# Kernel tuning notes

Measured on AMD Instinct MI355X. Metric: run time of the kernel, lower is better.

## Reference

```python
import jax, jax.numpy as jnp
import numpy as np

# network config (matches init_kwargs)
NI, NT, NA = 128, 3584, 384          # input / transmission / action neurons
N = NI + NT + NA                      # 4096 total neurons
HID, KQ, SIG = 32, 16, 16             # neuron_hidden_dim, key_query_dim, signal_dim
IN_DIM, OUT_DIM = 128, 64
B, T = 64, 32


def setup_inputs() -> dict:
    key = jax.random.key(0)
    ks = jax.random.split(key, 10)
    s = 0.1
    return {
        "x": jax.random.normal(ks[0], (B, T, IN_DIM), dtype=jnp.float32),
        # input neurons: MLP input_size -> HID -> SIG, stacked over NI neurons
        "W1_in": jax.random.normal(ks[1], (NI, HID, IN_DIM)) * s,
        "b1_in": jnp.zeros((NI, HID)),
        "W2_in": jax.random.normal(ks[2], (NI, SIG, HID)) * s,
        "b2_in": jnp.zeros((NI, SIG)),
        # transmission + action neurons: MLP SIG -> HID -> SIG, stacked over NT+NA
        "W1_o": jax.random.normal(ks[3], (NT + NA, HID, SIG)) * s,
        "b1_o": jnp.zeros((NT + NA, HID)),
        "W2_o": jax.random.normal(ks[4], (NT + NA, SIG, HID)) * s,
        "b2_o": jnp.zeros((NT + NA, SIG)),
        # per-neuron learned query / key vectors (broadcast over batch in original)
        "q_all": jax.random.normal(ks[5], (N, KQ)) * s,
        "k_all": jax.random.normal(ks[6], (N, KQ)) * s,
        # action projection: (NA*SIG) -> OUT_DIM
        "Wp": jax.random.normal(ks[7], (OUT_DIM, NA * SIG)) * s,
        "bp": jnp.zeros((OUT_DIM,)),
    }


def reference(x, W1_in, b1_in, W2_in, b2_in, W1_o, b1_o, W2_o, b2_o,
              q_all, k_all, Wp, bp):
    # attention weights are batch-independent (q/k are per-neuron params),
    # identical every step -> compute once. [N, N], softmax over keys.
    scores = (q_all @ k_all.T) / jnp.sqrt(jnp.asarray(KQ, x.dtype))
    attn = jax.nn.softmax(scores, axis=-1)

    def step(prev, x_t):
        # prev: [B, N, SIG]; aggregate messages from all neurons' previous outputs
        ctx = jnp.einsum('nm,bmd->bnd', attn, prev)              # [B, N, SIG]
        # input neurons all see the raw external input x_t
        h_in = jnp.tanh(jnp.einsum('bi,nhi->bnh', x_t, W1_in) + b1_in)
        out_in = jnp.einsum('bnh,ndh->bnd', h_in, W2_in) + b2_in  # [B, NI, SIG]
        # transmission + action neurons consume their attention context
        h_o = jnp.tanh(jnp.einsum('bns,nhs->bnh', ctx[:, NI:, :], W1_o) + b1_o)
        out_o = jnp.einsum('bnh,ndh->bnd', h_o, W2_o) + b2_o      # [B, NT+NA, SIG]
        new = jnp.concatenate([out_in, out_o], axis=1)            # [B, N, SIG]
        act = new[:, NI + NT:, :].reshape(x_t.shape[0], NA * SIG)
        y = act @ Wp.T + bp                                       # [B, OUT_DIM]
        return new, y

    prev0 = jnp.zeros((x.shape[0], N, SIG), dtype=x.dtype)
    _, ys = jax.lax.scan(step, prev0, jnp.swapaxes(x, 0, 1))      # [T, B, OUT]
    return jnp.swapaxes(ys, 0, 1)                                 # [B, T, OUT]
```

## Files before the change

kernel.cpp:

```cpp
#include <hip/hip_runtime.h>
#include <hip/hip_bf16.h>


#define NI 128
#define NTR 3584
#define NA 384
#define NN 4096
#define NO (NN - NI)
#define HID 32
#define KQ 16
#define SIG 16
#define IN_DIM 128
#define OUT_DIM 64
#define BB 64
#define TT 32
#define CDIM (BB * SIG)

#define BM 128
#define BN 128
#define BK 32
#define CTXP 132

typedef unsigned short ushort_t;
typedef __attribute__((ext_vector_type(8))) short short8v;
typedef __attribute__((ext_vector_type(4))) float f32x4;

__device__ inline ushort_t f2b(float f) {
  __hip_bfloat16 h = __float2bfloat16(f);
  return *reinterpret_cast<ushort_t*>(&h);
}

__device__ inline float tanh_fast(float s) {
  const float e = __expf(2.f * s);
  return 1.f - 2.f / (e + 1.f);
}

__device__ inline void gll16(const void* g, void* l) {
  __builtin_amdgcn_global_load_lds(
      (const __attribute__((address_space(1))) unsigned int*)g,
      (__attribute__((address_space(3))) unsigned int*)l, 16, 0, 0);
}

__global__ __launch_bounds__(256) void attn_kernel(const float* __restrict__ q_all,
                                                   const float* __restrict__ k_all,
                                                   ushort_t* __restrict__ A) {
  const int row = blockIdx.x;
  const int n = NI + row;
  float q[KQ];
#pragma unroll
  for (int i = 0; i < KQ; ++i) q[i] = q_all[n * KQ + i];

  float e[16];
  float local = 0.f;
#pragma unroll
  for (int j = 0; j < 16; ++j) {
    const int m = j * 256 + threadIdx.x;
    const float* kr = k_all + (size_t)m * KQ;
    float s = 0.f;
#pragma unroll
    for (int i = 0; i < KQ; ++i) s += q[i] * kr[i];
    e[j] = __expf(s * 0.25f);
    local += e[j];
  }
  __shared__ float red[256];
  red[threadIdx.x] = local;
  __syncthreads();
  for (int off = 128; off > 0; off >>= 1) {
    if (threadIdx.x < off) red[threadIdx.x] += red[threadIdx.x + off];
    __syncthreads();
  }
  const float inv = 1.f / red[0];
#pragma unroll
  for (int j = 0; j < 16; ++j) {
    const int m = j * 256 + threadIdx.x;
    A[(size_t)row * NN + m] = f2b(e[j] * inv);
  }
}

__global__ __launch_bounds__(256) void fused_step_kernel(
    const ushort_t* __restrict__ A,
    const ushort_t* __restrict__ Bst,
    const float* __restrict__ x, int t,
    const float* __restrict__ W1_in, const float* __restrict__ b1_in,
    const float* __restrict__ W2_in, const float* __restrict__ b2_in,
    const float* __restrict__ W1_o, const float* __restrict__ b1_o,
    const float* __restrict__ W2_o, const float* __restrict__ b2_o,
    ushort_t* __restrict__ STnext,
    float* __restrict__ act) {
  __shared__ ushort_t As[BM * BK];
  __shared__ ushort_t Bs[BN * BK];
  __shared__ float ctxs[128 * CTXP];

  const int tid = threadIdx.x;
  const int bx = blockIdx.x, by = blockIdx.y;
  const int nbase = by * BN;

  if (bx < 31) {
    const int mbase = bx * BM;
    const int wave = tid >> 6, lane = tid & 63;
    const int wr = wave >> 1, wc = wave & 1;

    f32x4 acc[4][4];
#pragma unroll
    for (int i = 0; i < 4; ++i)
#pragma unroll
      for (int j = 0; j < 4; ++j) acc[i][j] = (f32x4){0.f, 0.f, 0.f, 0.f};

    const int row0 = tid >> 2;
    const int k0 = (tid & 3) * 8;
    const ushort_t* ga0 = A + (size_t)(mbase + row0) * NN + k0;
    const ushort_t* ga1 = ga0 + (size_t)64 * NN;
    const ushort_t* gb0 = Bst + (size_t)(nbase + row0) * NN + k0;
    const ushort_t* gb1 = gb0 + (size_t)64 * NN;
    ushort_t* laA0 = As + wave * 512;
    ushort_t* laA1 = As + 2048 + wave * 512;
    ushort_t* laB0 = Bs + wave * 512;
    ushort_t* laB1 = Bs + 2048 + wave * 512;

    const int r = lane & 15, koff = (lane >> 4) * 8;

    for (int ks = 0; ks < NN / BK; ++ks) {
      __syncthreads();
      gll16(ga0, laA0); gll16(ga1, laA1);
      gll16(gb0, laB0); gll16(gb1, laB1);
      ga0 += BK; ga1 += BK; gb0 += BK; gb1 += BK;
      __syncthreads();

      short8v a[4], b[4];
#pragma unroll
      for (int mi = 0; mi < 4; ++mi)
        a[mi] = *(const short8v*)&As[(wr * 64 + mi * 16 + r) * BK + koff];
#pragma unroll
      for (int ni = 0; ni < 4; ++ni)
        b[ni] = *(const short8v*)&Bs[(wc * 64 + ni * 16 + r) * BK + koff];
#pragma unroll
      for (int mi = 0; mi < 4; ++mi)
#pragma unroll
        for (int ni = 0; ni < 4; ++ni)
          acc[mi][ni] = __builtin_amdgcn_mfma_f32_16x16x32_bf16(a[mi], b[ni], acc[mi][ni], 0, 0, 0);
    }

    const int r4 = (lane >> 4) * 4, cidx = lane & 15;
#pragma unroll
    for (int mi = 0; mi < 4; ++mi)
#pragma unroll
      for (int ni = 0; ni < 4; ++ni)
#pragma unroll
        for (int v = 0; v < 4; ++v)
          ctxs[(wr * 64 + mi * 16 + r4 + v) * CTXP + wc * 64 + ni * 16 + cidx] = acc[mi][ni][v];
    __syncthreads();

    const bool is_action = (mbase >= 3584);
    for (int iter = 0; iter < 4; ++iter) {
      const int nr = iter * 32 + (tid >> 3);
      const int bl = tid & 7;
      float cv[SIG];
      const float* cp = ctxs + nr * CTXP + bl * SIG;
#pragma unroll
      for (int d = 0; d < SIG; ++d) cv[d] = cp[d];

      const int no = mbase + nr;
      const float* w1 = W1_o + (size_t)no * HID * SIG;
      const float* b1 = b1_o + (size_t)no * HID;
      float h[HID];
#pragma unroll
      for (int hh = 0; hh < HID; ++hh) {
        float s = b1[hh];
#pragma unroll
        for (int d = 0; d < SIG; ++d) s += w1[hh * SIG + d] * cv[d];
        h[hh] = tanh_fast(s);
      }
      const float* w2 = W2_o + (size_t)no * SIG * HID;
      const float* b2 = b2_o + (size_t)no * SIG;
      float o16[SIG];
#pragma unroll
      for (int d = 0; d < SIG; ++d) {
        float s = b2[d];
#pragma unroll
        for (int hh = 0; hh < HID; ++hh) s += w2[d * HID + hh] * h[hh];
        o16[d] = s;
      }
      if (is_action) {
        float* ap = act + (size_t)(by * 8 + bl) * (NA * SIG) + (size_t)(no - 3584) * SIG;
#pragma unroll
        for (int k = 0; k < 4; ++k)
          *(float4*)(ap + 4 * k) = make_float4(o16[4*k], o16[4*k+1], o16[4*k+2], o16[4*k+3]);
      }
      float* wp = ctxs + nr * CTXP + bl * SIG;
#pragma unroll
      for (int d = 0; d < SIG; ++d) wp[d] = o16[d];
    }
    __syncthreads();
  } else {
    for (int iter = 0; iter < 4; ++iter) {
      const int nr = iter * 32 + (tid >> 3);
      const int bl = tid & 7;
      const int bg = by * 8 + bl;
      const float* xb = x + ((size_t)bg * TT + t) * IN_DIM;
      const float* w1 = W1_in + (size_t)nr * HID * IN_DIM;
      float h[HID];
#pragma unroll
      for (int hh = 0; hh < HID; ++hh) h[hh] = b1_in[nr * HID + hh];
      for (int i = 0; i < IN_DIM; i += 4) {
        const float4 xv = *(const float4*)(xb + i);
#pragma unroll
        for (int hh = 0; hh < HID; ++hh) {
          const float4 wv = *(const float4*)(w1 + hh * IN_DIM + i);
          h[hh] += wv.x * xv.x + wv.y * xv.y + wv.z * xv.z + wv.w * xv.w;
        }
      }
#pragma unroll
      for (int hh = 0; hh < HID; ++hh) h[hh] = tanh_fast(h[hh]);
      const float* w2 = W2_in + (size_t)nr * SIG * HID;
      float o16[SIG];
#pragma unroll
      for (int d = 0; d < SIG; ++d) {
        float s = b2_in[nr * SIG + d];
#pragma unroll
        for (int hh = 0; hh < HID; ++hh) s += w2[d * HID + hh] * h[hh];
        o16[d] = s;
      }
      float* wp = ctxs + nr * CTXP + bl * SIG;
#pragma unroll
      for (int d = 0; d < SIG; ++d) wp[d] = o16[d];
    }
    __syncthreads();
  }

  const int col0 = (bx == 31) ? 0 : NI + bx * BM;
  const int c = tid >> 1, nh = tid & 1;
  const float* colp = ctxs + (size_t)nh * 64 * CTXP + c;
  uint4* dst = (uint4*)(STnext + (size_t)(nbase + c) * NN + col0 + nh * 64);
#pragma unroll
  for (int k = 0; k < 8; ++k) {
    const unsigned w0 = (unsigned)f2b(colp[(k*8+0)*CTXP]) | ((unsigned)f2b(colp[(k*8+1)*CTXP]) << 16);
    const unsigned w1 = (unsigned)f2b(colp[(k*8+2)*CTXP]) | ((unsigned)f2b(colp[(k*8+3)*CTXP]) << 16);
    const unsigned w2 = (unsigned)f2b(colp[(k*8+4)*CTXP]) | ((unsigned)f2b(colp[(k*8+5)*CTXP]) << 16);
    const unsigned w3 = (unsigned)f2b(colp[(k*8+6)*CTXP]) | ((unsigned)f2b(colp[(k*8+7)*CTXP]) << 16);
    dst[k] = make_uint4(w0, w1, w2, w3);
  }
}

__global__ __launch_bounds__(256) void proj_kernel(const float* __restrict__ act,
                                                   const float* __restrict__ Wp,
                                                   const float* __restrict__ bp,
                                                   float* __restrict__ out, int t) {
  const int b = blockIdx.x;
  const int o = threadIdx.x & 63, q = threadIdx.x >> 6;
  const float* a = act + (size_t)b * (NA * SIG) + q * 1536;
  const float* w = Wp + (size_t)o * (NA * SIG) + q * 1536;
  float s = 0.f;
  for (int j = 0; j < 1536; j += 4) {
    const float4 av = *(const float4*)(a + j);
    const float4 wv = *(const float4*)(w + j);
    s += av.x * wv.x + av.y * wv.y + av.z * wv.z + av.w * wv.w;
  }
  __shared__ float red[4][64];
  red[q][o] = s;
  __syncthreads();
  if (q == 0) {
    const float y = red[0][o] + red[1][o] + red[2][o] + red[3][o] + bp[o];
    out[((size_t)b * TT + t) * OUT_DIM + o] = y;
  }
}

extern "C" void kernel_launch(void* const* d_in, const int* in_sizes, int n_in,
                              void* d_out, int out_size, void* d_ws, size_t ws_size,
                              hipStream_t stream) {
  const float* x     = (const float*)d_in[0];
  const float* W1_in = (const float*)d_in[1];
  const float* b1_in = (const float*)d_in[2];
  const float* W2_in = (const float*)d_in[3];
  const float* b2_in = (const float*)d_in[4];
  const float* W1_o  = (const float*)d_in[5];
  const float* b1_o  = (const float*)d_in[6];
  const float* W2_o  = (const float*)d_in[7];
  const float* b2_o  = (const float*)d_in[8];
  const float* q_all = (const float*)d_in[9];
  const float* k_all = (const float*)d_in[10];
  const float* Wp    = (const float*)d_in[11];
  const float* bp    = (const float*)d_in[12];
  float* out = (float*)d_out;

  char* p = (char*)d_ws;
  ushort_t* Abf = (ushort_t*)p; p += (size_t)NO * NN * 2;
  ushort_t* ST0 = (ushort_t*)p; p += (size_t)CDIM * NN * 2;
  ushort_t* ST1 = (ushort_t*)p; p += (size_t)CDIM * NN * 2;
  float*    act = (float*)p;    p += (size_t)BB * NA * SIG * 4;

  hipMemsetAsync(ST0, 0, (size_t)CDIM * NN * 2, stream);
  attn_kernel<<<NO, 256, 0, stream>>>(q_all, k_all, Abf);

  for (int t = 0; t < TT; ++t) {
    ushort_t* prev = (t & 1) ? ST1 : ST0;
    ushort_t* next = (t & 1) ? ST0 : ST1;
    dim3 grid(32, CDIM / BN);
    fused_step_kernel<<<grid, 256, 0, stream>>>(Abf, prev, x, t,
                                                W1_in, b1_in, W2_in, b2_in,
                                                W1_o, b1_o, W2_o, b2_o, next, act);
    proj_kernel<<<BB, 256, 0, stream>>>(act, Wp, bp, out, t);
  }
}
```

Measured before the change: 6.901 ms.

## Double-buffer GEMM K-tiles with swizzled LDS and transpose Wp for coalesced projection

The main GEMM loop now uses BK=64 with two LDS buffers, issuing the next tile's global-to-LDS loads before computing on the current one, so there is one barrier per step instead of two. Loads use an XOR swizzle on the k offset to reduce LDS bank conflicts. Separately, Wp is transposed once into workspace so the projection kernel reads weights coalesced across output lanes. In exchange, LDS use grows, with the ctx buffer plus double buffers at about 130KB, which may lower occupancy or exceed the limit.

```diff
diff --git a/kernel.cpp b/kernel.cpp
--- a/kernel.cpp
+++ b/kernel.cpp
@@ -18,7 +18,8 @@
 
 #define BM 128
 #define BN 128
-#define BK 32
+#define BK 64
+#define NKS (NN / BK)
 #define CTXP 132
 
 typedef unsigned short ushort_t;
@@ -75,6 +76,20 @@
     const int m = j * 256 + threadIdx.x;
     A[(size_t)row * NN + m] = f2b(e[j] * inv);
   }
+}
+
+__global__ __launch_bounds__(256) void wpt_kernel(const float* __restrict__ Wp,
+                                                  float* __restrict__ WpT) {
+  __shared__ float tile[64][65];
+  const int j0 = blockIdx.x * 64;
+  const int tx = threadIdx.x & 63, ty = threadIdx.x >> 6;
+#pragma unroll
+  for (int oo = ty; oo < 64; oo += 4)
+    tile[oo][tx] = Wp[(size_t)oo * (NA * SIG) + j0 + tx];
+  __syncthreads();
+#pragma unroll
+  for (int oo = ty; oo < 64; oo += 4)
+    WpT[(size_t)(j0 + oo) * 64 + tx] = tile[tx][oo];
 }
 
 __global__ __launch_bounds__(256) void fused_step_kernel(
@@ -87,8 +102,8 @@
     const float* __restrict__ W2_o, const float* __restrict__ b2_o,
     ushort_t* __restrict__ STnext,
     float* __restrict__ act) {
-  __shared__ ushort_t As[BM * BK];
-  __shared__ ushort_t Bs[BN * BK];
+  __shared__ ushort_t Abuf[2][BM * BK];
+  __shared__ ushort_t Bbuf[2][BN * BK];
   __shared__ float ctxs[128 * CTXP];
 
   const int tid = threadIdx.x;
@@ -99,6 +114,7 @@
     const int mbase = bx * BM;
     const int wave = tid >> 6, lane = tid & 63;
     const int wr = wave >> 1, wc = wave & 1;
+    const int r = lane & 15, hi = lane >> 4;
 
     f32x4 acc[4][4];
 #pragma unroll
@@ -106,41 +122,58 @@
 #pragma unroll
       for (int j = 0; j < 4; ++j) acc[i][j] = (f32x4){0.f, 0.f, 0.f, 0.f};
 
-    const int row0 = tid >> 2;
-    const int k0 = (tid & 3) * 8;
-    const ushort_t* ga0 = A + (size_t)(mbase + row0) * NN + k0;
-    const ushort_t* ga1 = ga0 + (size_t)64 * NN;
-    const ushort_t* gb0 = Bst + (size_t)(nbase + row0) * NN + k0;
-    const ushort_t* gb1 = gb0 + (size_t)64 * NN;
-    ushort_t* laA0 = As + wave * 512;
-    ushort_t* laA1 = As + 2048 + wave * 512;
-    ushort_t* laB0 = Bs + wave * 512;
-    ushort_t* laB1 = Bs + 2048 + wave * 512;
-
-    const int r = lane & 15, koff = (lane >> 4) * 8;
-
-    for (int ks = 0; ks < NN / BK; ++ks) {
-      __syncthreads();
-      gll16(ga0, laA0); gll16(ga1, laA1);
-      gll16(gb0, laB0); gll16(gb1, laB1);
-      ga0 += BK; ga1 += BK; gb0 += BK; gb1 += BK;
-      __syncthreads();
-
-      short8v a[4], b[4];
+    const int trow = tid >> 3;
+    const int k0 = ((tid & 7) ^ (trow & 7)) << 3;
+    const ushort_t* sa[4];
+    const ushort_t* sb[4];
+#pragma unroll
+    for (int c = 0; c < 4; ++c) {
+      sa[c] = A   + (size_t)(mbase + c * 32 + trow) * NN + k0;
+      sb[c] = Bst + (size_t)(nbase + c * 32 + trow) * NN + k0;
+    }
+    const int ldst = tid * 8;
+
+#pragma unroll
+    for (int c = 0; c < 4; ++c) {
+      gll16(sa[c], &Abuf[0][c * 2048 + ldst]);
+      gll16(sb[c], &Bbuf[0][c * 2048 + ldst]);
+      sa[c] += BK; sb[c] += BK;
+    }
+
+    for (int ks = 0; ks < NKS; ++ks) {
+      const int cur = ks & 1;
+      asm volatile("s_waitcnt vmcnt(0)" ::: "memory");
+      __builtin_amdgcn_s_barrier();
+      if (ks + 1 < NKS) {
+#pragma unroll
+        for (int c = 0; c < 4; ++c) {
+          gll16(sa[c], &Abuf[cur ^ 1][c * 2048 + ldst]);
+          gll16(sb[c], &Bbuf[cur ^ 1][c * 2048 + ldst]);
+          sa[c] += BK; sb[c] += BK;
+        }
+        asm volatile("" ::: "memory");
+      }
+
+      short8v a[4][2], b[4][2];
 #pragma unroll
       for (int mi = 0; mi < 4; ++mi)
-        a[mi] = *(const short8v*)&As[(wr * 64 + mi * 16 + r) * BK + koff];
-#pragma unroll
-      for (int ni = 0; ni < 4; ++ni)
-        b[ni] = *(const short8v*)&Bs[(wc * 64 + ni * 16 + r) * BK + koff];
+#pragma unroll
+        for (int kk = 0; kk < 2; ++kk) {
+          const int lb = kk * 64 + hi * 16;
+          const int sw = (lb ^ ((r & 7) << 4)) >> 1;
+          a[mi][kk] = *(const short8v*)&Abuf[cur][(wr * 64 + mi * 16 + r) * BK + sw];
+          b[mi][kk] = *(const short8v*)&Bbuf[cur][(wc * 64 + mi * 16 + r) * BK + sw];
+        }
 #pragma unroll
       for (int mi = 0; mi < 4; ++mi)
 #pragma unroll
-        for (int ni = 0; ni < 4; ++ni)
-          acc[mi][ni] = __builtin_amdgcn_mfma_f32_16x16x32_bf16(a[mi], b[ni], acc[mi][ni], 0, 0, 0);
-    }
-
-    const int r4 = (lane >> 4) * 4, cidx = lane & 15;
+        for (int ni = 0; ni < 4; ++ni) {
+          acc[mi][ni] = __builtin_amdgcn_mfma_f32_16x16x32_bf16(a[mi][0], b[ni][0], acc[mi][ni], 0, 0, 0);
+          acc[mi][ni] = __builtin_amdgcn_mfma_f32_16x16x32_bf16(a[mi][1], b[ni][1], acc[mi][ni], 0, 0, 0);
+        }
+    }
+
+    const int r4 = (hi) * 4, cidx = lane & 15;
 #pragma unroll
     for (int mi = 0; mi < 4; ++mi)
 #pragma unroll
@@ -242,18 +275,18 @@
 }
 
 __global__ __launch_bounds__(256) void proj_kernel(const float* __restrict__ act,
-                                                   const float* __restrict__ Wp,
+                                                   const float* __restrict__ WpT,
                                                    const float* __restrict__ bp,
                                                    float* __restrict__ out, int t) {
   const int b = blockIdx.x;
   const int o = threadIdx.x & 63, q = threadIdx.x >> 6;
   const float* a = act + (size_t)b * (NA * SIG) + q * 1536;
-  const float* w = Wp + (size_t)o * (NA * SIG) + q * 1536;
+  const float* w = WpT + (size_t)q * 1536 * 64 + o;
   float s = 0.f;
   for (int j = 0; j < 1536; j += 4) {
     const float4 av = *(const float4*)(a + j);
-    const float4 wv = *(const float4*)(w + j);
-    s += av.x * wv.x + av.y * wv.y + av.z * wv.z + av.w * wv.w;
+    s += av.x * w[(size_t)(j + 0) * 64] + av.y * w[(size_t)(j + 1) * 64]
+       + av.z * w[(size_t)(j + 2) * 64] + av.w * w[(size_t)(j + 3) * 64];
   }
   __shared__ float red[4][64];
   red[q][o] = s;
@@ -287,9 +320,11 @@
   ushort_t* ST0 = (ushort_t*)p; p += (size_t)CDIM * NN * 2;
   ushort_t* ST1 = (ushort_t*)p; p += (size_t)CDIM * NN * 2;
   float*    act = (float*)p;    p += (size_t)BB * NA * SIG * 4;
+  float*    WpT = (float*)p;    p += (size_t)NA * SIG * OUT_DIM * 4;
 
   hipMemsetAsync(ST0, 0, (size_t)CDIM * NN * 2, stream);
   attn_kernel<<<NO, 256, 0, stream>>>(q_all, k_all, Abf);
+  wpt_kernel<<<(NA * SIG) / 64, 256, 0, stream>>>(Wp, WpT);
 
   for (int t = 0; t < TT; ++t) {
     ushort_t* prev = (t & 1) ? ST1 : ST0;
@@ -298,6 +333,6 @@
     fused_step_kernel<<<grid, 256, 0, stream>>>(Abf, prev, x, t,
                                                 W1_in, b1_in, W2_in, b2_in,
                                                 W1_o, b1_o, W2_o, b2_o, next, act);
-    proj_kernel<<<BB, 256, 0, stream>>>(act, Wp, bp, out, t);
-  }
-}
+    proj_kernel<<<BB, 256, 0, stream>>>(act, WpT, bp, out, t);
+  }
+}
```

Measured after the change: 6.142 ms. -11.0%, faster.
